# Performance work log

Hardware: AMD Instinct MI355X
Metric: run time of the kernel (lower is better)

## Reference

```python
import jax, jax.numpy as jnp
import numpy as np

H = 2048      # hidden_size
E = 16        # num_experts
I = 512       # moe_intermediate_size
IS = 2048     # shared_expert_intermediate_size
TOP_K = 2
B, S = 1, 2048


def setup_inputs() -> dict:
    key = jax.random.key(0)
    ks = jax.random.split(key, 9)
    std = 0.02
    return {
        "hidden_states": jax.random.normal(ks[0], (B, S, H), dtype=jnp.float32),
        "gate_w": jax.random.normal(ks[1], (E, H), dtype=jnp.float32) * std,
        "w1": jax.random.normal(ks[2], (E, I, H), dtype=jnp.float32) * std,  # gate_proj per expert
        "w2": jax.random.normal(ks[3], (E, H, I), dtype=jnp.float32) * std,  # down_proj per expert
        "w3": jax.random.normal(ks[4], (E, I, H), dtype=jnp.float32) * std,  # up_proj per expert
        "ws_gate": jax.random.normal(ks[5], (IS, H), dtype=jnp.float32) * std,  # shared gate_proj
        "ws_up": jax.random.normal(ks[6], (IS, H), dtype=jnp.float32) * std,    # shared up_proj
        "ws_down": jax.random.normal(ks[7], (H, IS), dtype=jnp.float32) * std,  # shared down_proj
        "shared_gate_w": jax.random.normal(ks[8], (1, H), dtype=jnp.float32) * std,
    }


def reference(hidden_states, gate_w, w1, w2, w3, ws_gate, ws_up, ws_down, shared_gate_w):
    b, s, h = hidden_states.shape
    x = hidden_states.reshape(-1, h)                     # [T, H]
    T = x.shape[0]

    # Router: softmax in fp32, top-k, renormalize (norm_topk_prob=True)
    router_logits = x @ gate_w.T                         # [T, E]
    routing = jax.nn.softmax(router_logits.astype(jnp.float32), axis=-1)
    topw, sel = jax.lax.top_k(routing, TOP_K)            # [T, K]
    topw = topw / jnp.sum(topw, axis=-1, keepdims=True)
    topw = topw.astype(x.dtype)

    # Scatter top-k weights into dense [T, E] combine matrix (torch_moe semantics)
    combine = jnp.zeros((T, E), dtype=x.dtype).at[jnp.arange(T)[:, None], sel].set(topw)

    # Expert SwiGLU MLPs evaluated densely, masked/weighted by combine
    hmid = jax.nn.silu(jnp.einsum('th,eih->tei', x, w1)) * jnp.einsum('th,eih->tei', x, w3)  # [T,E,I]
    hmid = hmid * combine[:, :, None]
    moe_out = jnp.einsum('tei,ehi->th', hmid, w2)        # [T, H]

    # Shared expert with sigmoid gate
    shared = (jax.nn.silu(x @ ws_gate.T) * (x @ ws_up.T)) @ ws_down.T  # [T, H]
    shared = jax.nn.sigmoid(x @ shared_gate_w.T) * shared

    return (moe_out + shared).reshape(b, s, h)
```

## Files before the change

### kernel.cpp

```cpp
#include <hip/hip_runtime.h>
#include <cmath>

#define HDIM 2048
#define NEXP 16
#define IDIM 512
#define ISDIM 2048
#define NTOK 2048
#define MAXT 48
#define ROWSCAP (MAXT * 128)

#define GU_EXP (MAXT * 4)
#define GU_SH ((NTOK / 128) * (ISDIM / 128))
#define DN_SH ((NTOK / 128) * (HDIM / 256))
#define DN_EXP (MAXT * 8)

typedef short bf16x8 __attribute__((ext_vector_type(8)));
typedef float f32x4 __attribute__((ext_vector_type(4)));
typedef unsigned int u32x4 __attribute__((ext_vector_type(4)));
typedef unsigned short us;
typedef __attribute__((address_space(1))) const unsigned int* as1p;
typedef __attribute__((address_space(3))) unsigned int* as3p;

__device__ __forceinline__ us f2bf(float f) {
  unsigned int u = __builtin_bit_cast(unsigned int, f);
  u += 0x7FFFu + ((u >> 16) & 1u);
  return (us)(u >> 16);
}
__device__ __forceinline__ float bf2f(us v) {
  return __builtin_bit_cast(float, (unsigned)v << 16);
}

__device__ __forceinline__ void glds16(const void* g, void* l) {
  __builtin_amdgcn_global_load_lds((as1p)(unsigned long long)g,
                                   (as3p)(unsigned int)(unsigned long long)l, 16, 0, 0);
}

__device__ __forceinline__ void cvt8_nt(const unsigned* __restrict__ src,
                                        us* __restrict__ dst) {
  u32x4 a = __builtin_nontemporal_load((const u32x4*)src);
  u32x4 b = __builtin_nontemporal_load((const u32x4*)(src + 4));
  unsigned u0 = a.x + 0x8000u;
  unsigned u1 = a.y + 0x8000u;
  unsigned u2 = a.z + 0x8000u;
  unsigned u3 = a.w + 0x8000u;
  unsigned u4 = b.x + 0x8000u;
  unsigned u5 = b.y + 0x8000u;
  unsigned u6 = b.z + 0x8000u;
  unsigned u7 = b.w + 0x8000u;
  int4 v;
  v.x = __builtin_amdgcn_perm(u1, u0, 0x07060302);
  v.y = __builtin_amdgcn_perm(u3, u2, 0x07060302);
  v.z = __builtin_amdgcn_perm(u5, u4, 0x07060302);
  v.w = __builtin_amdgcn_perm(u7, u6, 0x07060302);
  *(int4*)dst = v;
}

__global__ __launch_bounds__(256) void k_cvt(
    const float* __restrict__ w1, const float* __restrict__ w2,
    const float* __restrict__ w3, const float* __restrict__ wsg,
    const float* __restrict__ wsu, const float* __restrict__ wsd,
    us* __restrict__ w1b, us* __restrict__ w2b, us* __restrict__ w3b,
    us* __restrict__ wsgb, us* __restrict__ wsub, us* __restrict__ wsdb) {
  int b = blockIdx.x;
  const float* src;
  us* dst;
  if (b < 1024) { src = w1; dst = w1b; }
  else if (b < 2048) { src = w2; dst = w2b; b -= 1024; }
  else if (b < 3072) { src = w3; dst = w3b; b -= 2048; }
  else if (b < 3328) { src = wsg; dst = wsgb; b -= 3072; }
  else if (b < 3584) { src = wsu; dst = wsub; b -= 3328; }
  else { src = wsd; dst = wsdb; b -= 3584; }
  size_t base = (size_t)b * 16384;
#pragma unroll
  for (int j = 0; j < 8; j++) {
    size_t off = base + ((size_t)j * 256 + threadIdx.x) * 8;
    cvt8_nt((const unsigned*)(src + off), dst + off);
  }
}

__global__ __launch_bounds__(256) void k_router(const float* __restrict__ x,
                                                const float* __restrict__ gate_w,
                                                const float* __restrict__ sgw,
                                                us* __restrict__ xb,
                                                int* __restrict__ sel,
                                                float* __restrict__ wnorm,
                                                float* __restrict__ sig,
                                                int* __restrict__ counts) {
  __shared__ float lg[4][17];
  __shared__ float L[17];
  int tid = threadIdx.x, wid = tid >> 6, lane = tid & 63;
  int t = blockIdx.x;
  const float4* xrow = reinterpret_cast<const float4*>(x + (size_t)t * HDIM);
  int i0 = wid * 128 + lane;
  float4 xv0 = xrow[i0], xv1 = xrow[i0 + 64];
  ushort4* xbrow = reinterpret_cast<ushort4*>(xb + (size_t)t * HDIM);
  ushort4 o0, o1;
  o0.x = f2bf(xv0.x); o0.y = f2bf(xv0.y); o0.z = f2bf(xv0.z); o0.w = f2bf(xv0.w);
  o1.x = f2bf(xv1.x); o1.y = f2bf(xv1.y); o1.z = f2bf(xv1.z); o1.w = f2bf(xv1.w);
  xbrow[i0] = o0;
  xbrow[i0 + 64] = o1;
  float acc[17];
#pragma unroll
  for (int e = 0; e < 17; e++) acc[e] = 0.f;
#pragma unroll
  for (int e = 0; e < 17; e++) {
    const float4* gr =
        reinterpret_cast<const float4*>(e < 16 ? gate_w + (size_t)e * HDIM : sgw);
    float4 g0 = gr[i0], g1 = gr[i0 + 64];
    acc[e] += xv0.x * g0.x + xv0.y * g0.y + xv0.z * g0.z + xv0.w * g0.w +
              xv1.x * g1.x + xv1.y * g1.y + xv1.z * g1.z + xv1.w * g1.w;
  }
#pragma unroll
  for (int off = 32; off; off >>= 1) {
#pragma unroll
    for (int e = 0; e < 17; e++) acc[e] += __shfl_xor(acc[e], off, 64);
  }
  if (lane == 0) {
#pragma unroll
    for (int e = 0; e < 17; e++) lg[wid][e] = acc[e];
  }
  __syncthreads();
  if (tid < 17) L[tid] = lg[0][tid] + lg[1][tid] + lg[2][tid] + lg[3][tid];
  __syncthreads();
  if (tid == 0) {
    int i1 = 0; float v1 = L[0];
#pragma unroll
    for (int i = 1; i < NEXP; i++) if (L[i] > v1) { v1 = L[i]; i1 = i; }
    int i2 = (i1 == 0) ? 1 : 0; float v2 = L[i2];
#pragma unroll
    for (int i = 0; i < NEXP; i++)
      if (i != i1 && i != i2 && L[i] > v2) { v2 = L[i]; i2 = i; }
    float wa = 1.f / (1.f + expf(v2 - v1));
    sel[2 * t] = i1; sel[2 * t + 1] = i2;
    wnorm[2 * t] = wa; wnorm[2 * t + 1] = 1.f - wa;
    sig[t] = 1.f / (1.f + expf(-L[16]));
    atomicAdd(&counts[i1], 1);
    atomicAdd(&counts[i2], 1);
  }
}

__global__ __launch_bounds__(64) void k_scatter(const int* __restrict__ counts,
                                                const int* __restrict__ sel,
                                                const float* __restrict__ wnorm,
                                                int* __restrict__ tile_expert,
                                                int* __restrict__ row_token,
                                                int* __restrict__ rowk,
                                                float* __restrict__ rw) {
  int e = blockIdx.x, lane = threadIdx.x;
  int base = 0, total = 0, nt_e = 0, cnt_e = 0;
  for (int i = 0; i < NEXP; i++) {
    int c = counts[i];
    int nt = (c + 127) >> 7;
    if (i == e) { base = total; cnt_e = c; nt_e = nt; }
    total += nt << 7;
  }
  for (int i = lane; i < nt_e; i += 64) tile_expert[(base >> 7) + i] = e;
  if (e == NEXP - 1)
    for (int m = (total >> 7) + lane; m < MAXT; m += 64) tile_expert[m] = -1;
  for (int r = cnt_e + lane; r < nt_e * 128; r += 64) row_token[base + r] = -1;
  int run = 0;
  for (int t0 = 0; t0 < NTOK; t0 += 64) {
    int t = t0 + lane;
    int s0 = sel[2 * t], s1 = sel[2 * t + 1];
    int k = (s1 == e) ? 1 : 0;
    bool m = (s0 == e) || (s1 == e);
    unsigned long long mask = __ballot(m);
    int rank = __popcll(mask & ((1ull << lane) - 1ull));
    if (m) {
      int row = base + run + rank;
      row_token[row] = t;
      rowk[row] = k;
      rw[row] = wnorm[2 * t + k];
    }
    run += __popcll(mask);
  }
}

__global__ __launch_bounds__(512) void k_gu(
    const us* __restrict__ xb, const us* __restrict__ w1b,
    const us* __restrict__ w3b, const us* __restrict__ wsgb,
    const us* __restrict__ wsub, const int* __restrict__ tile_expert,
    const int* __restrict__ row_token, us* __restrict__ hmid,
    us* __restrict__ hs) {
  __shared__ us As[128 * 64];
  __shared__ us Bs[2][128 * 64];
  __shared__ int toks_s[128];
  int bid = blockIdx.x, tid = threadIdx.x;
  int w = tid >> 6, lane = tid & 63;
  const us *bG, *bU;
  us* outp;
  int mt, n0, ostride;
  if (bid < GU_EXP) {
    mt = bid >> 2; int nt = bid & 3;
    int e = tile_expert[mt];
    if (e < 0) return;
    if (tid < 128) {
      int tk = row_token[mt * 128 + tid];
      toks_s[tid] = tk < 0 ? 0 : tk;
    }
    bG = w1b + ((size_t)e * IDIM + nt * 128) * HDIM;
    bU = w3b + ((size_t)e * IDIM + nt * 128) * HDIM;
    outp = hmid; ostride = IDIM; n0 = nt * 128;
  } else {
    int sb = bid - GU_EXP;
    mt = sb >> 4; int nt = sb & 15;
    if (tid < 128) toks_s[tid] = mt * 128 + tid;
    bG = wsgb + (size_t)(nt * 128) * HDIM;
    bU = wsub + (size_t)(nt * 128) * HDIM;
    outp = hs; ostride = ISDIM; n0 = nt * 128;
  }
  __syncthreads();
  int lr = lane >> 3, lc = lane & 7;
  int swz = (lc ^ lr) * 8;
  const us* aSrc0 = xb + (size_t)toks_s[w * 16 + lr] * HDIM + swz;
  const us* aSrc1 = xb + (size_t)toks_s[w * 16 + 8 + lr] * HDIM + swz;
  int mat = w >> 2, sub = w & 3, wm = sub >> 1, wn = sub & 1;
  const us* bSrc = (mat ? bU : bG) + (size_t)(sub * 32 + lr) * HDIM + swz;
  us* bDst = &Bs[mat][sub * 32 * 64];
  int quad = lane >> 4, l16 = lane & 15, sw = l16 & 7;
  f32x4 acc[4][4] = {};
  for (int k0 = 0; k0 < HDIM; k0 += 64) {
    glds16(aSrc0 + k0, As + w * 1024);
    glds16(aSrc1 + k0, As + w * 1024 + 512);
#pragma unroll
    for (int g = 0; g < 4; g++)
      glds16(bSrc + (size_t)(g * 8) * HDIM + k0, bDst + g * 512);
    __syncthreads();
#pragma unroll
    for (int ks = 0; ks < 2; ks++) {
      int cb = (ks * 4 + quad) ^ sw;
      bf16x8 af[4], bf[4];
#pragma unroll
      for (int ms = 0; ms < 4; ms++)
        af[ms] = *(const bf16x8*)&As[((wm * 64 + ms * 16 + l16) * 8 + cb) * 8];
#pragma unroll
      for (int ns = 0; ns < 4; ns++)
        bf[ns] = *(const bf16x8*)&Bs[mat][((wn * 64 + ns * 16 + l16) * 8 + cb) * 8];
#pragma unroll
      for (int ms = 0; ms < 4; ms++)
#pragma unroll
        for (int ns = 0; ns < 4; ns++)
          acc[ms][ns] = __builtin_amdgcn_mfma_f32_16x16x32_bf16(af[ms], bf[ns], acc[ms][ns], 0, 0, 0);
    }
    __syncthreads();
  }
  us* ub = (us*)Bs;
  if (mat == 1) {
#pragma unroll
    for (int ms = 0; ms < 4; ms++)
#pragma unroll
      for (int ns = 0; ns < 4; ns++)
#pragma unroll
        for (int r = 0; r < 4; r++) {
          int row = wm * 64 + ms * 16 + quad * 4 + r;
          int col = wn * 64 + ns * 16 + l16;
          ub[row * 128 + col] = f2bf(acc[ms][ns][r]);
        }
  }
  __syncthreads();
  if (mat == 0) {
#pragma unroll
    for (int ms = 0; ms < 4; ms++)
#pragma unroll
      for (int ns = 0; ns < 4; ns++)
#pragma unroll
        for (int r = 0; r < 4; r++) {
          int row = wm * 64 + ms * 16 + quad * 4 + r;
          int col = wn * 64 + ns * 16 + l16;
          float g = acc[ms][ns][r];
          float u = bf2f(ub[row * 128 + col]);
          float hv = (g / (1.f + __expf(-g))) * u;
          outp[(size_t)(mt * 128 + row) * ostride + n0 + col] = f2bf(hv);
        }
  }
}

__global__ __launch_bounds__(512) void k_down(
    const us* __restrict__ hmid, const us* __restrict__ hs,
    const us* __restrict__ w2b, const us* __restrict__ wsdb,
    const int* __restrict__ tile_expert, const int* __restrict__ row_token,
    const int* __restrict__ rowk, const float* __restrict__ rw,
    const float* __restrict__ sig, us* __restrict__ slab) {
  __shared__ us As[128 * 64];
  __shared__ us Bs[256 * 64];
  __shared__ int idx_s[128];
  __shared__ float wgt_s[128];
  int bid = blockIdx.x, tid = threadIdx.x;
  int w = tid >> 6, lane = tid & 63;
  const us* aBase;
  const us* bBase;
  int K, mt, n0;
  if (bid < DN_SH) {
    mt = bid >> 3; int nt = bid & 7;
    aBase = hs + (size_t)mt * 128 * ISDIM; K = ISDIM;
    bBase = wsdb + (size_t)(nt * 256) * ISDIM;
    n0 = nt * 256;
    if (tid < 128) {
      int t = mt * 128 + tid;
      idx_s[tid] = 2 * NTOK * HDIM + t * HDIM;
      wgt_s[tid] = sig[t];
    }
  } else {
    int sb = bid - DN_SH;
    mt = sb >> 3; int nt = sb & 7;
    int e = tile_expert[mt];
    if (e < 0) return;
    aBase = hmid + (size_t)mt * 128 * IDIM; K = IDIM;
    bBase = w2b + ((size_t)e * HDIM + nt * 256) * IDIM;
    n0 = nt * 256;
    if (tid < 128) {
      int tk = row_token[mt * 128 + tid];
      if (tk < 0) { idx_s[tid] = -1; wgt_s[tid] = 0.f; }
      else {
        idx_s[tid] = (rowk[mt * 128 + tid] * NTOK + tk) * HDIM;
        wgt_s[tid] = rw[mt * 128 + tid];
      }
    }
  }
  __syncthreads();
  int lr = lane >> 3, lc = lane & 7;
  int swz = (lc ^ lr) * 8;
  const us* aSrc0 = aBase + (size_t)(w * 16 + lr) * K + swz;
  const us* aSrc1 = aBase + (size_t)(w * 16 + 8 + lr) * K + swz;
  const us* bSrc = bBase + (size_t)(w * 32 + lr) * K + swz;
  us* bDst = Bs + w * 32 * 64;
  int wmn = w >> 2, wn = w & 3;
  int quad = lane >> 4, l16 = lane & 15, sw = l16 & 7;
  f32x4 acc[4][4] = {};
  for (int k0 = 0; k0 < K; k0 += 64) {
    glds16(aSrc0 + k0, As + w * 1024);
    glds16(aSrc1 + k0, As + w * 1024 + 512);
#pragma unroll
    for (int g = 0; g < 4; g++)
      glds16(bSrc + (size_t)(g * 8) * K + k0, bDst + g * 512);
    __syncthreads();
#pragma unroll
    for (int ks = 0; ks < 2; ks++) {
      int cb = (ks * 4 + quad) ^ sw;
      bf16x8 af[4], bf[4];
#pragma unroll
      for (int ms = 0; ms < 4; ms++)
        af[ms] = *(const bf16x8*)&As[((wmn * 64 + ms * 16 + l16) * 8 + cb) * 8];
#pragma unroll
      for (int ns = 0; ns < 4; ns++)
        bf[ns] = *(const bf16x8*)&Bs[((wn * 64 + ns * 16 + l16) * 8 + cb) * 8];
#pragma unroll
      for (int ms = 0; ms < 4; ms++)
#pragma unroll
        for (int ns = 0; ns < 4; ns++)
          acc[ms][ns] = __builtin_amdgcn_mfma_f32_16x16x32_bf16(af[ms], bf[ns], acc[ms][ns], 0, 0, 0);
    }
    __syncthreads();
  }
#pragma unroll
  for (int ms = 0; ms < 4; ms++)
#pragma unroll
    for (int r = 0; r < 4; r++) {
      int rr = wmn * 64 + ms * 16 + quad * 4 + r;
      int ix = idx_s[rr];
      if (ix >= 0) {
        float wgt = wgt_s[rr];
        us* orow = slab + (size_t)ix + n0 + wn * 64;
#pragma unroll
        for (int ns = 0; ns < 4; ns++)
          orow[ns * 16 + l16] = f2bf(wgt * acc[ms][ns][r]);
      }
    }
}

__global__ __launch_bounds__(256) void k_combine(const us* __restrict__ slab,
                                                 float* __restrict__ out) {
  size_t i = ((size_t)blockIdx.x * 256 + threadIdx.x) * 8;
  bf16x8 a = __builtin_nontemporal_load((const bf16x8*)(slab + i));
  bf16x8 b = __builtin_nontemporal_load((const bf16x8*)(slab + (size_t)NTOK * HDIM + i));
  bf16x8 c = __builtin_nontemporal_load((const bf16x8*)(slab + 2 * (size_t)NTOK * HDIM + i));
  f32x4 o0, o1;
#pragma unroll
  for (int j = 0; j < 4; j++)
    o0[j] = bf2f((us)a[j]) + bf2f((us)b[j]) + bf2f((us)c[j]);
#pragma unroll
  for (int j = 0; j < 4; j++)
    o1[j] = bf2f((us)a[4 + j]) + bf2f((us)b[4 + j]) + bf2f((us)c[4 + j]);
  __builtin_nontemporal_store(o0, (f32x4*)(out + i));
  __builtin_nontemporal_store(o1, (f32x4*)(out + i + 4));
}

extern "C" void kernel_launch(void* const* d_in, const int* in_sizes, int n_in,
                              void* d_out, int out_size, void* d_ws, size_t ws_size,
                              hipStream_t stream) {
  const float* x = (const float*)d_in[0];
  const float* gate_w = (const float*)d_in[1];
  const float* w1 = (const float*)d_in[2];
  const float* w2 = (const float*)d_in[3];
  const float* w3 = (const float*)d_in[4];
  const float* wsg = (const float*)d_in[5];
  const float* wsu = (const float*)d_in[6];
  const float* wsd = (const float*)d_in[7];
  const float* sgw = (const float*)d_in[8];
  float* out = (float*)d_out;

  us* xb = (us*)d_ws;
  us* hs = xb + (size_t)NTOK * HDIM;
  us* hmid = hs + (size_t)NTOK * ISDIM;
  us* slab = hmid + (size_t)ROWSCAP * IDIM;
  us* w1b = slab + (size_t)3 * NTOK * HDIM;
  us* w3b = w1b + (size_t)NEXP * IDIM * HDIM;
  us* w2b = w3b + (size_t)NEXP * IDIM * HDIM;
  us* wsgb = w2b + (size_t)NEXP * HDIM * IDIM;
  us* wsub = wsgb + (size_t)ISDIM * HDIM;
  us* wsdb = wsub + (size_t)ISDIM * HDIM;
  float* rw = (float*)(wsdb + (size_t)HDIM * ISDIM);
  float* wnorm = rw + ROWSCAP;
  float* sig = wnorm + 2 * NTOK;
  int* sel = (int*)(sig + NTOK);
  int* row_token = sel + 2 * NTOK;
  int* rowk = row_token + ROWSCAP;
  int* counts = rowk + ROWSCAP;
  int* tile_expert = counts + NEXP;

  hipMemsetAsync(counts, 0, NEXP * sizeof(int), stream);
  k_cvt<<<dim3(3840), dim3(256), 0, stream>>>(w1, w2, w3, wsg, wsu, wsd,
                                              w1b, w2b, w3b, wsgb, wsub, wsdb);
  k_router<<<dim3(NTOK), dim3(256), 0, stream>>>(x, gate_w, sgw, xb, sel, wnorm,
                                                 sig, counts);
  k_scatter<<<dim3(NEXP), dim3(64), 0, stream>>>(counts, sel, wnorm, tile_expert,
                                                 row_token, rowk, rw);
  k_gu<<<dim3(GU_EXP + GU_SH), dim3(512), 0, stream>>>(
      xb, w1b, w3b, wsgb, wsub, tile_expert, row_token, hmid, hs);
  k_down<<<dim3(DN_SH + DN_EXP), dim3(512), 0, stream>>>(
      hmid, hs, w2b, wsdb, tile_expert, row_token, rowk, rw, sig, slab);
  k_combine<<<dim3(NTOK * HDIM / 2048), dim3(256), 0, stream>>>(slab, out);
}
```

Baseline: 419.1 us.

## Accumulate down-proj results into output with atomics, drop combine kernel

The down-projection kernel now adds its weighted fp32 results straight into the zeroed output with atomicAdd, instead of writing three bf16 slabs that a separate combine kernel then sums. This removes the slab buffer, the rowk array and one kernel launch, along with the slab write and read traffic. In exchange it adds a memset of the output and three scattered fp32 atomic adds per output element, and the order of the floating-point sums is no longer fixed.

```diff
diff --git a/kernel.cpp b/kernel.cpp
--- a/kernel.cpp
+++ b/kernel.cpp
@@ -144,7 +144,6 @@
                                                 const float* __restrict__ wnorm,
                                                 int* __restrict__ tile_expert,
                                                 int* __restrict__ row_token,
-                                                int* __restrict__ rowk,
                                                 float* __restrict__ rw) {
   int e = blockIdx.x, lane = threadIdx.x;
   int base = 0, total = 0, nt_e = 0, cnt_e = 0;
@@ -169,7 +168,6 @@
     if (m) {
       int row = base + run + rank;
       row_token[row] = t;
-      rowk[row] = k;
       rw[row] = wnorm[2 * t + k];
     }
     run += __popcll(mask);
@@ -279,11 +277,11 @@
     const us* __restrict__ hmid, const us* __restrict__ hs,
     const us* __restrict__ w2b, const us* __restrict__ wsdb,
     const int* __restrict__ tile_expert, const int* __restrict__ row_token,
-    const int* __restrict__ rowk, const float* __restrict__ rw,
-    const float* __restrict__ sig, us* __restrict__ slab) {
+    const float* __restrict__ rw, const float* __restrict__ sig,
+    float* __restrict__ out) {
   __shared__ us As[128 * 64];
   __shared__ us Bs[256 * 64];
-  __shared__ int idx_s[128];
+  __shared__ int tok_s[128];
   __shared__ float wgt_s[128];
   int bid = blockIdx.x, tid = threadIdx.x;
   int w = tid >> 6, lane = tid & 63;
@@ -297,7 +295,7 @@
     n0 = nt * 256;
     if (tid < 128) {
       int t = mt * 128 + tid;
-      idx_s[tid] = 2 * NTOK * HDIM + t * HDIM;
+      tok_s[tid] = t;
       wgt_s[tid] = sig[t];
     }
   } else {
@@ -310,11 +308,8 @@
     n0 = nt * 256;
     if (tid < 128) {
       int tk = row_token[mt * 128 + tid];
-      if (tk < 0) { idx_s[tid] = -1; wgt_s[tid] = 0.f; }
-      else {
-        idx_s[tid] = (rowk[mt * 128 + tid] * NTOK + tk) * HDIM;
-        wgt_s[tid] = rw[mt * 128 + tid];
-      }
+      tok_s[tid] = tk;
+      wgt_s[tid] = tk < 0 ? 0.f : rw[mt * 128 + tid];
     }
   }
   __syncthreads();
@@ -357,32 +352,15 @@
 #pragma unroll
     for (int r = 0; r < 4; r++) {
       int rr = wmn * 64 + ms * 16 + quad * 4 + r;
-      int ix = idx_s[rr];
-      if (ix >= 0) {
+      int tok = tok_s[rr];
+      if (tok >= 0) {
         float wgt = wgt_s[rr];
-        us* orow = slab + (size_t)ix + n0 + wn * 64;
+        float* orow = out + (size_t)tok * HDIM + n0 + wn * 64;
 #pragma unroll
         for (int ns = 0; ns < 4; ns++)
-          orow[ns * 16 + l16] = f2bf(wgt * acc[ms][ns][r]);
+          atomicAdd(&orow[ns * 16 + l16], wgt * acc[ms][ns][r]);
       }
     }
-}
-
-__global__ __launch_bounds__(256) void k_combine(const us* __restrict__ slab,
-                                                 float* __restrict__ out) {
-  size_t i = ((size_t)blockIdx.x * 256 + threadIdx.x) * 8;
-  bf16x8 a = __builtin_nontemporal_load((const bf16x8*)(slab + i));
-  bf16x8 b = __builtin_nontemporal_load((const bf16x8*)(slab + (size_t)NTOK * HDIM + i));
-  bf16x8 c = __builtin_nontemporal_load((const bf16x8*)(slab + 2 * (size_t)NTOK * HDIM + i));
-  f32x4 o0, o1;
-#pragma unroll
-  for (int j = 0; j < 4; j++)
-    o0[j] = bf2f((us)a[j]) + bf2f((us)b[j]) + bf2f((us)c[j]);
-#pragma unroll
-  for (int j = 0; j < 4; j++)
-    o1[j] = bf2f((us)a[4 + j]) + bf2f((us)b[4 + j]) + bf2f((us)c[4 + j]);
-  __builtin_nontemporal_store(o0, (f32x4*)(out + i));
-  __builtin_nontemporal_store(o1, (f32x4*)(out + i + 4));
 }
 
 extern "C" void kernel_launch(void* const* d_in, const int* in_sizes, int n_in,
@@ -402,8 +380,7 @@
   us* xb = (us*)d_ws;
   us* hs = xb + (size_t)NTOK * HDIM;
   us* hmid = hs + (size_t)NTOK * ISDIM;
-  us* slab = hmid + (size_t)ROWSCAP * IDIM;
-  us* w1b = slab + (size_t)3 * NTOK * HDIM;
+  us* w1b = hmid + (size_t)ROWSCAP * IDIM;
   us* w3b = w1b + (size_t)NEXP * IDIM * HDIM;
   us* w2b = w3b + (size_t)NEXP * IDIM * HDIM;
   us* wsgb = w2b + (size_t)NEXP * HDIM * IDIM;
@@ -414,20 +391,19 @@
   float* sig = wnorm + 2 * NTOK;
   int* sel = (int*)(sig + NTOK);
   int* row_token = sel + 2 * NTOK;
-  int* rowk = row_token + ROWSCAP;
-  int* counts = rowk + ROWSCAP;
+  int* counts = row_token + ROWSCAP;
   int* tile_expert = counts + NEXP;
 
   hipMemsetAsync(counts, 0, NEXP * sizeof(int), stream);
+  hipMemsetAsync(out, 0, (size_t)NTOK * HDIM * sizeof(float), stream);
   k_cvt<<<dim3(3840), dim3(256), 0, stream>>>(w1, w2, w3, wsg, wsu, wsd,
                                               w1b, w2b, w3b, wsgb, wsub, wsdb);
   k_router<<<dim3(NTOK), dim3(256), 0, stream>>>(x, gate_w, sgw, xb, sel, wnorm,
                                                  sig, counts);
   k_scatter<<<dim3(NEXP), dim3(64), 0, stream>>>(counts, sel, wnorm, tile_expert,
-                                                 row_token, rowk, rw);
+                                                 row_token, rw);
   k_gu<<<dim3(GU_EXP + GU_SH), dim3(512), 0, stream>>>(
       xb, w1b, w3b, wsgb, wsub, tile_expert, row_token, hmid, hs);
   k_down<<<dim3(DN_SH + DN_EXP), dim3(512), 0, stream>>>(
-      hmid, hs, w2b, wsdb, tile_expert, row_token, rowk, rw, sig, slab);
-  k_combine<<<dim3(NTOK * HDIM / 2048), dim3(256), 0, stream>>>(slab, out);
-}
+      hmid, hs, w2b, wsdb, tile_expert, row_token, rw, sig, out);
+}
```

After: 435.2 us. 3.8% more time.
